# Kernel tuning notes

Measured on AMD Instinct MI355X. Metric: run time of the kernel, lower is better.

Reference implementation:

```python
import jax, jax.numpy as jnp
import numpy as np

NEG_SLOPE = 0.2
EPS = 1e-16
N_NODES, N_EDGES, N_GRAPHS = 50000, 800000, 64
EMB, HID, HEADS = 128, 64, 4


def segment_softmax(scores, seg, num_segments):
    # scores: [E, H], seg: [E] destination ids
    m = jax.ops.segment_max(scores, seg, num_segments=num_segments)
    e = jnp.exp(scores - m[seg])
    s = jax.ops.segment_sum(e, seg, num_segments=num_segments)
    return e / (s[seg] + EPS)


def gat_layer(x, edge_index, W, att_src, att_dst, bias, heads, out_ch, num_nodes):
    # PyG GATConv (add_self_loops handled by caller): linear -> per-edge attn -> segment softmax -> scatter-add
    h = (x @ W).reshape(num_nodes, heads, out_ch)          # [N, H, C]
    a_src = jnp.sum(h * att_src, axis=-1)                  # [N, H]
    a_dst = jnp.sum(h * att_dst, axis=-1)                  # [N, H]
    src, dst = edge_index[0], edge_index[1]
    alpha = jax.nn.leaky_relu(a_src[src] + a_dst[dst], NEG_SLOPE)   # [E, H]
    alpha = segment_softmax(alpha, dst, num_nodes)
    msg = h[src] * alpha[:, :, None]                       # [E, H, C]
    out = jax.ops.segment_sum(msg, dst, num_segments=num_nodes)
    return out.reshape(num_nodes, heads * out_ch) + bias


def setup_inputs() -> dict:
    key = jax.random.key(0)
    ks = jax.random.split(key, 16)
    g = lambda k, shape, fan: jax.random.normal(k, shape, jnp.float32) * (1.0 / np.sqrt(fan))
    x = jax.random.normal(ks[0], (N_NODES, EMB), jnp.float32)
    edge_index = jax.random.randint(ks[1], (2, N_EDGES), 0, N_NODES, dtype=jnp.int64)
    batch_map = jnp.sort(jax.random.randint(ks[2], (N_NODES,), 0, N_GRAPHS, dtype=jnp.int64))
    return {
        'x': x, 'edge_index': edge_index, 'batch_map': batch_map,
        'W1': g(ks[3], (EMB, HEADS * HID), EMB),
        'att_src1': g(ks[4], (HEADS, HID), HID),
        'att_dst1': g(ks[5], (HEADS, HID), HID),
        'b1': jnp.zeros((HEADS * HID,), jnp.float32),
        'W2': g(ks[6], (HEADS * HID, HID), HEADS * HID),
        'att_src2': g(ks[7], (1, HID), HID),
        'att_dst2': g(ks[8], (1, HID), HID),
        'b2': jnp.zeros((HID,), jnp.float32),
        'Wg1': g(ks[9], (HID, HID), HID),
        'bg1': jnp.zeros((HID,), jnp.float32),
        'Wg2': g(ks[10], (HID, 1), HID),
        'bg2': jnp.zeros((1,), jnp.float32),
    }


def reference(x, edge_index, batch_map, W1, att_src1, att_dst1, b1, W2, att_src2, att_dst2, b2, Wg1, bg1, Wg2, bg2):
    n = x.shape[0]
    # GATConv default add_self_loops=True
    loops = jnp.arange(n, dtype=edge_index.dtype)
    ei = jnp.concatenate([edge_index, jnp.stack([loops, loops])], axis=1)
    h = jax.nn.elu(gat_layer(x, ei, W1, att_src1, att_dst1, b1, HEADS, HID, n))
    h = jax.nn.elu(gat_layer(h, ei, W2, att_src2, att_dst2, b2, 1, HID, n))
    # AttentionalAggregation: gate MLP -> segment softmax over graphs -> weighted sum
    gate = jax.nn.relu(h @ Wg1 + bg1) @ Wg2 + bg2          # [N, 1]
    w = segment_softmax(gate, batch_map, N_GRAPHS)         # [N, 1]
    graph_emb = jax.ops.segment_sum(w * h, batch_map, num_segments=N_GRAPHS)
    return graph_emb
```

## Files before the change

### kernel.cpp

```cpp
#include <hip/hip_runtime.h>
#include <math.h>

#define N_NODES 50000
#define N_EDGES 800000
#define E_TOT   850000
#define N_GRAPHS 64
#define EMB 128
#define HID 64
#define HEADS 4
#define NEG_SLOPE 0.2f
#define EPS 1e-16f
#define MAX_DEG 64
#define G1_TILES (N_NODES / 16)
#define ELL_BLKS ((E_TOT + 255) / 256)

typedef short bf16x8 __attribute__((ext_vector_type(8)));
typedef float f32x4  __attribute__((ext_vector_type(4)));

__device__ __forceinline__ float leaky(float x) { return x >= 0.f ? x : NEG_SLOPE * x; }
__device__ __forceinline__ float elu(float x)   { return x > 0.f ? x : expf(x) - 1.f; }

__device__ __forceinline__ unsigned short f2bf(float f) {
    unsigned u = __float_as_uint(f);
    return (unsigned short)((u + 0x7FFFu + ((u >> 16) & 1u)) >> 16);
}
__device__ __forceinline__ float bf2f(unsigned short h) {
    return __uint_as_float((unsigned)h << 16);
}

__device__ __forceinline__ void edge_sd(const int* __restrict__ ei, int e, int& s, int& d) {
    if (e < N_EDGES) { s = ei[e]; d = ei[N_EDGES + e]; }
    else             { s = d = e - N_EDGES; }
}

__device__ __forceinline__ int lbound(const int* __restrict__ a, int n, int v) {
    int lo = 0, hi = n;
    while (lo < hi) { int mid = (lo + hi) >> 1; if (a[mid] < v) lo = mid + 1; else hi = mid; }
    return lo;
}

__global__ void k_wprep(const float* __restrict__ W1, const float* __restrict__ as1, const float* __restrict__ ad1,
                        const float* __restrict__ W2, const float* __restrict__ as2, const float* __restrict__ ad2,
                        const float* __restrict__ Wg1,
                        unsigned short* __restrict__ W1t, float* __restrict__ v1s, float* __restrict__ v1d,
                        unsigned short* __restrict__ W2t, float* __restrict__ v2s, float* __restrict__ v2d,
                        unsigned short* __restrict__ wg1h, unsigned short* __restrict__ wg1l,
                        unsigned* __restrict__ cnt) {
    int b = blockIdx.x, t = threadIdx.x;
    if (b < 32) {
        for (int i = b * 1024 + t; i < (b + 1) * 1024; i += 256) {
            int c = i >> 7, k = i & 127;
            W1t[i] = f2bf(W1[k * 256 + c]);
        }
    } else if (b < 48) {
        int bb = b - 32;
        for (int i = bb * 1024 + t; i < (bb + 1) * 1024; i += 256) {
            int c = i >> 8, k = i & 255;
            W2t[i] = f2bf(W2[k * 64 + c]);
        }
    } else if (b == 48) {
        for (int i = t; i < 512; i += 256) {
            int h = i >> 7, k = i & 127;
            float s = 0.f, d = 0.f;
            for (int c = 0; c < 64; ++c) {
                float wv = W1[k * 256 + h * 64 + c];
                s = fmaf(wv, as1[h * 64 + c], s);
                d = fmaf(wv, ad1[h * 64 + c], d);
            }
            v1s[i] = s; v1d[i] = d;
        }
    } else if (b == 49) {
        float s = 0.f, d = 0.f;
        for (int cc = 0; cc < 64; ++cc) {
            float wv = W2[t * 64 + cc];
            s = fmaf(wv, as2[cc], s);
            d = fmaf(wv, ad2[cc], d);
        }
        v2s[t] = s; v2d[t] = d;
    } else if (b == 50) {
        for (int i = t; i < 4096; i += 256) {
            int c = i >> 6, k = i & 63;
            float v = Wg1[k * 64 + c];
            unsigned short h = f2bf(v);
            wg1h[i] = h;
            wg1l[i] = f2bf(v - bf2f(h));
        }
    } else {
        for (int i = (b - 51) * 256 + t; i < N_NODES; i += 13 * 256) cnt[i] = 0;
    }
}

__global__ __launch_bounds__(256)
void k_prep2(const float* __restrict__ x, const unsigned short* __restrict__ W1t,
             const float* __restrict__ v1s, const float* __restrict__ v1d,
             unsigned short* __restrict__ h1b, float* __restrict__ a_src1,
             float* __restrict__ a_dst1,
             const int* __restrict__ ei, unsigned* __restrict__ cnt,
             unsigned short* __restrict__ ell) {
    if (blockIdx.x >= G1_TILES) {
        int e = (blockIdx.x - G1_TILES) * 256 + threadIdx.x;
        if (e < E_TOT) {
            int s, d; edge_sd(ei, e, s, d);
            unsigned slot = atomicAdd(&cnt[d], 1u);
            if (slot < MAX_DEG) ell[d * MAX_DEG + slot] = (unsigned short)s;
        }
        return;
    }
    int w = threadIdx.x >> 6, l = threadIdx.x & 63;
    int r = l & 15, kg = l >> 4;
    int tile = blockIdx.x;
    const float* xr = x + (size_t)(tile * 16 + r) * 128 + kg * 8;
    bf16x8 af[4];
    float ps = 0.f, pd = 0.f;
    #pragma unroll
    for (int j = 0; j < 4; ++j) {
        float4 f0 = *(const float4*)(xr + j * 32);
        float4 f1 = *(const float4*)(xr + j * 32 + 4);
        const float* vs = v1s + w * 128 + j * 32 + kg * 8;
        const float* vd = v1d + w * 128 + j * 32 + kg * 8;
        float4 s0 = *(const float4*)vs, s1 = *(const float4*)(vs + 4);
        float4 d0 = *(const float4*)vd, d1 = *(const float4*)(vd + 4);
        ps += f0.x*s0.x + f0.y*s0.y + f0.z*s0.z + f0.w*s0.w
            + f1.x*s1.x + f1.y*s1.y + f1.z*s1.z + f1.w*s1.w;
        pd += f0.x*d0.x + f0.y*d0.y + f0.z*d0.z + f0.w*d0.w
            + f1.x*d1.x + f1.y*d1.y + f1.z*d1.z + f1.w*d1.w;
        bf16x8 t;
        t[0] = (short)f2bf(f0.x); t[1] = (short)f2bf(f0.y);
        t[2] = (short)f2bf(f0.z); t[3] = (short)f2bf(f0.w);
        t[4] = (short)f2bf(f1.x); t[5] = (short)f2bf(f1.y);
        t[6] = (short)f2bf(f1.z); t[7] = (short)f2bf(f1.w);
        af[j] = t;
    }
    ps += __shfl_xor(ps, 16); ps += __shfl_xor(ps, 32);
    pd += __shfl_xor(pd, 16); pd += __shfl_xor(pd, 32);
    if (l < 16) {
        a_src1[(size_t)(tile * 16 + r) * 4 + w] = ps;
        a_dst1[(size_t)(tile * 16 + r) * 4 + w] = pd;
    }
    for (int cc = 0; cc < 4; ++cc) {
        int c0 = cc * 64 + w * 16;
        const bf16x8* B = (const bf16x8*)(W1t + (size_t)(c0 + r) * 128 + kg * 8);
        f32x4 acc = {0.f, 0.f, 0.f, 0.f};
        acc = __builtin_amdgcn_mfma_f32_16x16x32_bf16(af[0], B[0],  acc, 0, 0, 0);
        acc = __builtin_amdgcn_mfma_f32_16x16x32_bf16(af[1], B[4],  acc, 0, 0, 0);
        acc = __builtin_amdgcn_mfma_f32_16x16x32_bf16(af[2], B[8],  acc, 0, 0, 0);
        acc = __builtin_amdgcn_mfma_f32_16x16x32_bf16(af[3], B[12], acc, 0, 0, 0);
        #pragma unroll
        for (int j = 0; j < 4; ++j)
            h1b[(size_t)(tile * 16 + kg * 4 + j) * 256 + c0 + r] = f2bf(acc[j]);
    }
}

__global__ __launch_bounds__(1024)
void k_layer1(const unsigned short* __restrict__ ell, const unsigned* __restrict__ cnt,
              const float4* __restrict__ asrc, const float4* __restrict__ adst,
              const unsigned short* __restrict__ h1b, const float4* __restrict__ bias,
              const float4* __restrict__ v2s4, const float4* __restrict__ v2d4,
              const unsigned short* __restrict__ W2t,
              float* __restrict__ a_src2, float* __restrict__ a_dst2,
              unsigned short* __restrict__ h2b) {
    __shared__ float sw[4][16][65];
    __shared__ int   ss[16][MAX_DEG];
    __shared__ unsigned short Ash[16][264];
    int wave = threadIdx.x >> 6, lane = threadIdx.x & 63;
    int node = blockIdx.x * 16 + wave;
    int deg = min((int)cnt[node], MAX_DEG);

    float4 ad = adst[node];
    float a0 = -INFINITY, a1 = -INFINITY, a2 = -INFINITY, a3 = -INFINITY;
    int s = 0;
    if (lane < deg) {
        s = ell[node * MAX_DEG + lane];
        float4 as = asrc[s];
        a0 = leaky(as.x + ad.x); a1 = leaky(as.y + ad.y);
        a2 = leaky(as.z + ad.z); a3 = leaky(as.w + ad.w);
    }
    float m0 = a0, m1 = a1, m2 = a2, m3 = a3;
    for (int o = 32; o > 0; o >>= 1) {
        m0 = fmaxf(m0, __shfl_xor(m0, o)); m1 = fmaxf(m1, __shfl_xor(m1, o));
        m2 = fmaxf(m2, __shfl_xor(m2, o)); m3 = fmaxf(m3, __shfl_xor(m3, o));
    }
    float w0 = lane < deg ? expf(a0 - m0) : 0.f;
    float w1 = lane < deg ? expf(a1 - m1) : 0.f;
    float w2 = lane < deg ? expf(a2 - m2) : 0.f;
    float w3 = lane < deg ? expf(a3 - m3) : 0.f;
    float t0 = w0, t1 = w1, t2 = w2, t3 = w3;
    for (int o = 32; o > 0; o >>= 1) {
        t0 += __shfl_xor(t0, o); t1 += __shfl_xor(t1, o);
        t2 += __shfl_xor(t2, o); t3 += __shfl_xor(t3, o);
    }
    w0 /= (t0 + EPS); w1 /= (t1 + EPS); w2 /= (t2 + EPS); w3 /= (t3 + EPS);
    if (lane < deg) {
        sw[0][wave][lane] = w0; sw[1][wave][lane] = w1;
        sw[2][wave][lane] = w2; sw[3][wave][lane] = w3;
        ss[wave][lane] = s;
    }
    int head = lane >> 4;
    float c0 = 0.f, c1 = 0.f, c2 = 0.f, c3 = 0.f;
    ushort4 hcur = *(const ushort4*)(h1b + (size_t)ss[wave][0] * 256 + lane * 4);
    float   wcur = sw[head][wave][0];
    for (int e = 1; e < deg; ++e) {
        ushort4 hnx = *(const ushort4*)(h1b + (size_t)ss[wave][e] * 256 + lane * 4);
        float   wnx = sw[head][wave][e];
        c0 = fmaf(bf2f(hcur.x), wcur, c0); c1 = fmaf(bf2f(hcur.y), wcur, c1);
        c2 = fmaf(bf2f(hcur.z), wcur, c2); c3 = fmaf(bf2f(hcur.w), wcur, c3);
        hcur = hnx; wcur = wnx;
    }
    c0 = fmaf(bf2f(hcur.x), wcur, c0); c1 = fmaf(bf2f(hcur.y), wcur, c1);
    c2 = fmaf(bf2f(hcur.z), wcur, c2); c3 = fmaf(bf2f(hcur.w), wcur, c3);

    float4 b = bias[lane];
    float o0 = elu(c0 + b.x), o1 = elu(c1 + b.y), o2 = elu(c2 + b.z), o3 = elu(c3 + b.w);
    *(ushort4*)&Ash[wave][lane * 4] = make_ushort4(f2bf(o0), f2bf(o1), f2bf(o2), f2bf(o3));
    float4 vs = v2s4[lane], vd = v2d4[lane];
    float ps = o0 * vs.x + o1 * vs.y + o2 * vs.z + o3 * vs.w;
    float pd = o0 * vd.x + o1 * vd.y + o2 * vd.z + o3 * vd.w;
    for (int o = 32; o > 0; o >>= 1) { ps += __shfl_xor(ps, o); pd += __shfl_xor(pd, o); }
    if (lane == 0) { a_src2[node] = ps; a_dst2[node] = pd; }

    __syncthreads();
    if (wave < 4) {
        int r = lane & 15, kg = lane >> 4;
        f32x4 acc = {0.f, 0.f, 0.f, 0.f};
        #pragma unroll
        for (int kk = 0; kk < 8; ++kk) {
            bf16x8 afr = *(const bf16x8*)&Ash[r][kg * 8 + kk * 32];
            bf16x8 bfr = *(const bf16x8*)(W2t + (size_t)(wave * 16 + r) * 256 + kg * 8 + kk * 32);
            acc = __builtin_amdgcn_mfma_f32_16x16x32_bf16(afr, bfr, acc, 0, 0, 0);
        }
        #pragma unroll
        for (int j = 0; j < 4; ++j)
            h2b[(size_t)(blockIdx.x * 16 + kg * 4 + j) * 64 + wave * 16 + r] = f2bf(acc[j]);
    }
}

__global__ __launch_bounds__(1024)
void k_layer2(const unsigned short* __restrict__ ell, const unsigned* __restrict__ cnt,
              const float* __restrict__ asrc, const float* __restrict__ adst,
              const unsigned short* __restrict__ h2b, const float* __restrict__ bias,
              const unsigned short* __restrict__ wg1h, const unsigned short* __restrict__ wg1l,
              const float* __restrict__ bg1, const float* __restrict__ Wg2,
              const float* __restrict__ bg2,
              float* __restrict__ out2, float* __restrict__ gate) {
    __shared__ float sw[16][MAX_DEG];
    __shared__ int   ss[16][MAX_DEG];
    __shared__ unsigned short Ah[16][72], Al[16][72];
    __shared__ float gp[4][16];
    int wave = threadIdx.x >> 6, lane = threadIdx.x & 63;
    int half = lane >> 5, li = lane & 31;
    int node = blockIdx.x * 16 + wave;
    int deg = min((int)cnt[node], MAX_DEG);

    float adv = adst[node];
    float a = -INFINITY;
    int s = 0;
    if (lane < deg) {
        s = ell[node * MAX_DEG + lane];
        a = leaky(asrc[s] + adv);
    }
    float m = a;
    for (int o = 32; o > 0; o >>= 1) m = fmaxf(m, __shfl_xor(m, o));
    float w = lane < deg ? expf(a - m) : 0.f;
    float t = w;
    for (int o = 32; o > 0; o >>= 1) t += __shfl_xor(t, o);
    w /= (t + EPS);
    if (lane < deg) { sw[wave][lane] = w; ss[wave][lane] = s; }

    float c0 = 0.f, c1 = 0.f;
    int row = half;
    unsigned ucur = 0; float wcur = 0.f;
    if (row < deg) {
        ucur = *(const unsigned*)(h2b + (size_t)ss[wave][row] * 64 + li * 2);
        wcur = sw[wave][row];
    }
    while (row < deg) {
        int nrow = row + 2;
        unsigned unx = 0; float wnx = 0.f;
        if (nrow < deg) {
            unx = *(const unsigned*)(h2b + (size_t)ss[wave][nrow] * 64 + li * 2);
            wnx = sw[wave][nrow];
        }
        c0 = fmaf(__uint_as_float(ucur << 16), wcur, c0);
        c1 = fmaf(__uint_as_float(ucur & 0xffff0000u), wcur, c1);
        ucur = unx; wcur = wnx; row = nrow;
    }
    c0 += __shfl_xor(c0, 32);
    c1 += __shfl_xor(c1, 32);
    if (half == 0) {
        float o0 = elu(c0 + bias[li * 2]);
        float o1 = elu(c1 + bias[li * 2 + 1]);
        *(float2*)(out2 + (size_t)node * 64 + li * 2) = make_float2(o0, o1);
        unsigned short h0 = f2bf(o0), h1 = f2bf(o1);
        *(unsigned*)&Ah[wave][li * 2] = ((unsigned)h1 << 16) | h0;
        unsigned short l0 = f2bf(o0 - bf2f(h0)), l1 = f2bf(o1 - bf2f(h1));
        *(unsigned*)&Al[wave][li * 2] = ((unsigned)l1 << 16) | l0;
    }

    __syncthreads();
    if (wave < 4) {
        int r = lane & 15, kg = lane >> 4;
        const bf16x8* Bh = (const bf16x8*)(wg1h + (size_t)(wave * 16 + r) * 64 + kg * 8);
        const bf16x8* Bl = (const bf16x8*)(wg1l + (size_t)(wave * 16 + r) * 64 + kg * 8);
        bf16x8 ah0 = *(const bf16x8*)&Ah[r][kg * 8];
        bf16x8 ah1 = *(const bf16x8*)&Ah[r][kg * 8 + 32];
        bf16x8 al0 = *(const bf16x8*)&Al[r][kg * 8];
        bf16x8 al1 = *(const bf16x8*)&Al[r][kg * 8 + 32];
        f32x4 acc = {0.f, 0.f, 0.f, 0.f};
        acc = __builtin_amdgcn_mfma_f32_16x16x32_bf16(ah0, Bh[0], acc, 0, 0, 0);
        acc = __builtin_amdgcn_mfma_f32_16x16x32_bf16(ah1, Bh[4], acc, 0, 0, 0);
        acc = __builtin_amdgcn_mfma_f32_16x16x32_bf16(ah0, Bl[0], acc, 0, 0, 0);
        acc = __builtin_amdgcn_mfma_f32_16x16x32_bf16(ah1, Bl[4], acc, 0, 0, 0);
        acc = __builtin_amdgcn_mfma_f32_16x16x32_bf16(al0, Bh[0], acc, 0, 0, 0);
        acc = __builtin_amdgcn_mfma_f32_16x16x32_bf16(al1, Bh[4], acc, 0, 0, 0);
        int col = wave * 16 + r;
        float wg2 = Wg2[col], bb = bg1[col];
        float part[4];
        #pragma unroll
        for (int j = 0; j < 4; ++j) part[j] = fmaxf(acc[j] + bb, 0.f) * wg2;
        #pragma unroll
        for (int o = 8; o > 0; o >>= 1) {
            #pragma unroll
            for (int j = 0; j < 4; ++j) part[j] += __shfl_xor(part[j], o);
        }
        if (r == 0) {
            #pragma unroll
            for (int j = 0; j < 4; ++j) gp[wave][kg * 4 + j] = part[j];
        }
    }
    __syncthreads();
    if (threadIdx.x < 16)
        gate[blockIdx.x * 16 + threadIdx.x] = gp[0][threadIdx.x] + gp[1][threadIdx.x]
                                            + gp[2][threadIdx.x] + gp[3][threadIdx.x] + bg2[0];
}

__global__ __launch_bounds__(1024)
void k_final(const float* __restrict__ gate, const float* __restrict__ hfin,
             const int* __restrict__ batch, float* __restrict__ out) {
    __shared__ float red[16];
    __shared__ float redc[16][64];
    int g = blockIdx.x;
    int lo = lbound(batch, N_NODES, g);
    int hi = lbound(batch, N_NODES, g + 1);
    int tid = threadIdx.x, wave = tid >> 6, lane = tid & 63;

    float m = -INFINITY;
    for (int i = lo + tid; i < hi; i += 1024) m = fmaxf(m, gate[i]);
    for (int o = 32; o > 0; o >>= 1) m = fmaxf(m, __shfl_xor(m, o));
    if (lane == 0) red[wave] = m;
    __syncthreads();
    m = -INFINITY;
    #pragma unroll
    for (int i = 0; i < 16; ++i) m = fmaxf(m, red[i]);
    __syncthreads();

    float s = 0.f;
    for (int i = lo + tid; i < hi; i += 1024) s += expf(gate[i] - m);
    for (int o = 32; o > 0; o >>= 1) s += __shfl_xor(s, o);
    if (lane == 0) red[wave] = s;
    __syncthreads();
    s = 0.f;
    #pragma unroll
    for (int i = 0; i < 16; ++i) s += red[i];

    float acc = 0.f;
    for (int i = lo + wave; i < hi; i += 16)
        acc = fmaf(expf(gate[i] - m), hfin[(size_t)i * 64 + lane], acc);
    redc[wave][lane] = acc;
    __syncthreads();
    if (tid < 64) {
        float r = 0.f;
        #pragma unroll
        for (int i = 0; i < 16; ++i) r += redc[i][tid];
        out[g * 64 + tid] = r / (s + EPS);
    }
}

extern "C" void kernel_launch(void* const* d_in, const int* in_sizes, int n_in,
                              void* d_out, int out_size, void* d_ws, size_t ws_size,
                              hipStream_t stream) {
    const float* x    = (const float*)d_in[0];
    const int*   ei   = (const int*)d_in[1];
    const int*   batch= (const int*)d_in[2];
    const float* W1   = (const float*)d_in[3];
    const float* as1  = (const float*)d_in[4];
    const float* ad1  = (const float*)d_in[5];
    const float* b1   = (const float*)d_in[6];
    const float* W2   = (const float*)d_in[7];
    const float* as2  = (const float*)d_in[8];
    const float* ad2  = (const float*)d_in[9];
    const float* b2   = (const float*)d_in[10];
    const float* Wg1  = (const float*)d_in[11];
    const float* bg1  = (const float*)d_in[12];
    const float* Wg2  = (const float*)d_in[13];
    const float* bg2  = (const float*)d_in[14];
    float* out = (float*)d_out;

    char* W = (char*)d_ws;
    size_t off = 0;
    unsigned* cnt = (unsigned*)(W + off); off += (size_t)N_NODES * 4;
    unsigned short* ell  = (unsigned short*)(W + off); off += (size_t)N_NODES * MAX_DEG * 2;
    unsigned short* h1b  = (unsigned short*)(W + off); off += (size_t)N_NODES * 256 * 2;
    float* a_src1 = (float*)(W + off); off += (size_t)N_NODES * HEADS * 4;
    float* a_dst1 = (float*)(W + off); off += (size_t)N_NODES * HEADS * 4;
    float* a_src2 = (float*)(W + off); off += (size_t)N_NODES * 4;
    float* a_dst2 = (float*)(W + off); off += (size_t)N_NODES * 4;
    float* out2   = (float*)(W + off); off += (size_t)N_NODES * HID * 4;
    float* gate   = (float*)(W + off); off += (size_t)N_NODES * 4;
    unsigned short* W1t = (unsigned short*)(W + off); off += (size_t)128 * 256 * 2;
    float* v1s = (float*)(W + off); off += 512 * 4;
    float* v1d = (float*)(W + off); off += 512 * 4;
    unsigned short* W2t = (unsigned short*)(W + off); off += (size_t)64 * 256 * 2;
    float* v2s = (float*)(W + off); off += 256 * 4;
    float* v2d = (float*)(W + off); off += 256 * 4;
    unsigned short* wg1h = (unsigned short*)(W + off); off += (size_t)64 * 64 * 2;
    unsigned short* wg1l = (unsigned short*)(W + off); off += (size_t)64 * 64 * 2;
    unsigned short* h2b = (unsigned short*)(W + off); off += (size_t)N_NODES * HID * 2;
    (void)ws_size; (void)in_sizes; (void)n_in; (void)out_size;

    k_wprep<<<64, 256, 0, stream>>>(W1, as1, ad1, W2, as2, ad2, Wg1,
                                    W1t, v1s, v1d, W2t, v2s, v2d, wg1h, wg1l, cnt);
    k_prep2<<<G1_TILES + ELL_BLKS, 256, 0, stream>>>(x, W1t, v1s, v1d, h1b, a_src1, a_dst1,
                                                     ei, cnt, ell);
    k_layer1<<<N_NODES / 16, 1024, 0, stream>>>(ell, cnt, (const float4*)a_src1,
        (const float4*)a_dst1, h1b, (const float4*)b1,
        (const float4*)v2s, (const float4*)v2d, W2t, a_src2, a_dst2, h2b);
    k_layer2<<<N_NODES / 16, 1024, 0, stream>>>(ell, cnt, a_src2, a_dst2, h2b, b2,
                                                wg1h, wg1l, bg1, Wg2, bg2, out2, gate);
    k_final<<<N_GRAPHS, 1024, 0, stream>>>(gate, out2, batch, out);
}
```

Measured before the change: 282.6 us.

## Build ELL adjacency with per-block LDS atomics over owned node ranges

The ELL neighbour-list build moves out of the fused GEMM/scatter kernel into a dedicated kernel with 64 blocks. Each block owns a contiguous slice of destination nodes, scans every edge's destination, and claims slots with shared-memory atomics instead of global atomics. Self-loops are written directly as slot 0, so the separate zeroing of the global count array goes away. The cost is that every block reads the whole destination array and only 64 blocks run, which underuses the GPU; the ELL build also no longer overlaps with the first GEMM.

```diff
diff --git a/kernel.cpp b/kernel.cpp
--- a/kernel.cpp
+++ b/kernel.cpp
@@ -11,8 +11,8 @@
 #define NEG_SLOPE 0.2f
 #define EPS 1e-16f
 #define MAX_DEG 64
-#define G1_TILES (N_NODES / 16)
-#define ELL_BLKS ((E_TOT + 255) / 256)
+#define ELL_NB 64
+#define ELL_NODES ((N_NODES + ELL_NB - 1) / ELL_NB)
 
 typedef short bf16x8 __attribute__((ext_vector_type(8)));
 typedef float f32x4  __attribute__((ext_vector_type(4)));
@@ -26,17 +26,38 @@
 }
 __device__ __forceinline__ float bf2f(unsigned short h) {
     return __uint_as_float((unsigned)h << 16);
-}
-
-__device__ __forceinline__ void edge_sd(const int* __restrict__ ei, int e, int& s, int& d) {
-    if (e < N_EDGES) { s = ei[e]; d = ei[N_EDGES + e]; }
-    else             { s = d = e - N_EDGES; }
 }
 
 __device__ __forceinline__ int lbound(const int* __restrict__ a, int n, int v) {
     int lo = 0, hi = n;
     while (lo < hi) { int mid = (lo + hi) >> 1; if (a[mid] < v) lo = mid + 1; else hi = mid; }
     return lo;
+}
+
+__global__ __launch_bounds__(1024)
+void k_ell2(const int* __restrict__ ei, unsigned* __restrict__ cnt,
+            unsigned short* __restrict__ ell) {
+    __shared__ unsigned lcnt[ELL_NODES];
+    int base = blockIdx.x * ELL_NODES;
+    int nOwn = min(base + ELL_NODES, N_NODES) - base;
+    for (int i = threadIdx.x; i < nOwn; i += 1024) {
+        lcnt[i] = 1;
+        ell[(size_t)(base + i) * MAX_DEG] = (unsigned short)(base + i);
+    }
+    __syncthreads();
+    const int* dsts = ei + N_EDGES;
+    for (int e = threadIdx.x; e < N_EDGES; e += 1024) {
+        int d = dsts[e];
+        unsigned rel = (unsigned)(d - base);
+        if (rel < (unsigned)nOwn) {
+            unsigned slot = atomicAdd(&lcnt[rel], 1u);
+            if (slot < MAX_DEG)
+                ell[(size_t)d * MAX_DEG + slot] = (unsigned short)ei[e];
+        }
+    }
+    __syncthreads();
+    for (int i = threadIdx.x; i < nOwn; i += 1024)
+        cnt[base + i] = lcnt[i];
 }
 
 __global__ void k_wprep(const float* __restrict__ W1, const float* __restrict__ as1, const float* __restrict__ ad1,
@@ -44,8 +65,7 @@
                         const float* __restrict__ Wg1,
                         unsigned short* __restrict__ W1t, float* __restrict__ v1s, float* __restrict__ v1d,
                         unsigned short* __restrict__ W2t, float* __restrict__ v2s, float* __restrict__ v2d,
-                        unsigned short* __restrict__ wg1h, unsigned short* __restrict__ wg1l,
-                        unsigned* __restrict__ cnt) {
+                        unsigned short* __restrict__ wg1h, unsigned short* __restrict__ wg1l) {
     int b = blockIdx.x, t = threadIdx.x;
     if (b < 32) {
         for (int i = b * 1024 + t; i < (b + 1) * 1024; i += 256) {
@@ -77,7 +97,7 @@
             d = fmaf(wv, ad2[cc], d);
         }
         v2s[t] = s; v2d[t] = d;
-    } else if (b == 50) {
+    } else {
         for (int i = t; i < 4096; i += 256) {
             int c = i >> 6, k = i & 63;
             float v = Wg1[k * 64 + c];
@@ -85,27 +105,14 @@
             wg1h[i] = h;
             wg1l[i] = f2bf(v - bf2f(h));
         }
-    } else {
-        for (int i = (b - 51) * 256 + t; i < N_NODES; i += 13 * 256) cnt[i] = 0;
     }
 }
 
 __global__ __launch_bounds__(256)
-void k_prep2(const float* __restrict__ x, const unsigned short* __restrict__ W1t,
-             const float* __restrict__ v1s, const float* __restrict__ v1d,
-             unsigned short* __restrict__ h1b, float* __restrict__ a_src1,
-             float* __restrict__ a_dst1,
-             const int* __restrict__ ei, unsigned* __restrict__ cnt,
-             unsigned short* __restrict__ ell) {
-    if (blockIdx.x >= G1_TILES) {
-        int e = (blockIdx.x - G1_TILES) * 256 + threadIdx.x;
-        if (e < E_TOT) {
-            int s, d; edge_sd(ei, e, s, d);
-            unsigned slot = atomicAdd(&cnt[d], 1u);
-            if (slot < MAX_DEG) ell[d * MAX_DEG + slot] = (unsigned short)s;
-        }
-        return;
-    }
+void k_gemm1_mfma(const float* __restrict__ x, const unsigned short* __restrict__ W1t,
+                  const float* __restrict__ v1s, const float* __restrict__ v1d,
+                  unsigned short* __restrict__ h1b, float* __restrict__ a_src1,
+                  float* __restrict__ a_dst1) {
     int w = threadIdx.x >> 6, l = threadIdx.x & 63;
     int r = l & 15, kg = l >> 4;
     int tile = blockIdx.x;
@@ -417,10 +424,10 @@
     unsigned short* h2b = (unsigned short*)(W + off); off += (size_t)N_NODES * HID * 2;
     (void)ws_size; (void)in_sizes; (void)n_in; (void)out_size;
 
-    k_wprep<<<64, 256, 0, stream>>>(W1, as1, ad1, W2, as2, ad2, Wg1,
-                                    W1t, v1s, v1d, W2t, v2s, v2d, wg1h, wg1l, cnt);
-    k_prep2<<<G1_TILES + ELL_BLKS, 256, 0, stream>>>(x, W1t, v1s, v1d, h1b, a_src1, a_dst1,
-                                                     ei, cnt, ell);
+    k_ell2<<<ELL_NB, 1024, 0, stream>>>(ei, cnt, ell);
+    k_wprep<<<51, 256, 0, stream>>>(W1, as1, ad1, W2, as2, ad2, Wg1,
+                                    W1t, v1s, v1d, W2t, v2s, v2d, wg1h, wg1l);
+    k_gemm1_mfma<<<N_NODES / 16, 256, 0, stream>>>(x, W1t, v1s, v1d, h1b, a_src1, a_dst1);
     k_layer1<<<N_NODES / 16, 1024, 0, stream>>>(ell, cnt, (const float4*)a_src1,
         (const float4*)a_dst1, h1b, (const float4*)b1,
         (const float4*)v2s, (const float4*)v2d, W2t, a_src2, a_dst2, h2b);
```

Result: slower. 579.9 us (+105.2%).

## Split per-node edge counters into four sub-buckets and compact into ELL

Applied to the files above, without the earlier changes.

Edges are spread over four sub-counters per destination node, chosen by edge index mod 4, so atomic contention on each counter drops. A new compaction kernel then merges the sub-buckets into the dense ELL layout. This adds an extra kernel launch, more workspace traffic and a larger zero-init. Each sub-bucket is capped at 20 entries, so a node whose edges are unevenly spread can drop edges that the single 64-slot counter would have kept.

```diff
diff --git a/kernel.cpp b/kernel.cpp
--- a/kernel.cpp
+++ b/kernel.cpp
@@ -11,6 +11,7 @@
 #define NEG_SLOPE 0.2f
 #define EPS 1e-16f
 #define MAX_DEG 64
+#define SUB_CAP 20
 #define G1_TILES (N_NODES / 16)
 #define ELL_BLKS ((E_TOT + 255) / 256)
 
@@ -45,7 +46,7 @@
                         unsigned short* __restrict__ W1t, float* __restrict__ v1s, float* __restrict__ v1d,
                         unsigned short* __restrict__ W2t, float* __restrict__ v2s, float* __restrict__ v2d,
                         unsigned short* __restrict__ wg1h, unsigned short* __restrict__ wg1l,
-                        unsigned* __restrict__ cnt) {
+                        unsigned* __restrict__ cnt4) {
     int b = blockIdx.x, t = threadIdx.x;
     if (b < 32) {
         for (int i = b * 1024 + t; i < (b + 1) * 1024; i += 256) {
@@ -86,7 +87,7 @@
             wg1l[i] = f2bf(v - bf2f(h));
         }
     } else {
-        for (int i = (b - 51) * 256 + t; i < N_NODES; i += 13 * 256) cnt[i] = 0;
+        for (int i = (b - 51) * 256 + t; i < 4 * N_NODES; i += 13 * 256) cnt4[i] = 0;
     }
 }
 
@@ -95,14 +96,16 @@
              const float* __restrict__ v1s, const float* __restrict__ v1d,
              unsigned short* __restrict__ h1b, float* __restrict__ a_src1,
              float* __restrict__ a_dst1,
-             const int* __restrict__ ei, unsigned* __restrict__ cnt,
-             unsigned short* __restrict__ ell) {
+             const int* __restrict__ ei, unsigned* __restrict__ cnt4,
+             unsigned short* __restrict__ ell4) {
     if (blockIdx.x >= G1_TILES) {
         int e = (blockIdx.x - G1_TILES) * 256 + threadIdx.x;
         if (e < E_TOT) {
             int s, d; edge_sd(ei, e, s, d);
-            unsigned slot = atomicAdd(&cnt[d], 1u);
-            if (slot < MAX_DEG) ell[d * MAX_DEG + slot] = (unsigned short)s;
+            int sub = e & 3;
+            unsigned slot = atomicAdd(&cnt4[sub * N_NODES + d], 1u);
+            if (slot < SUB_CAP)
+                ell4[(size_t)d * (4 * SUB_CAP) + sub * SUB_CAP + slot] = (unsigned short)s;
         }
         return;
     }
@@ -151,6 +154,24 @@
     }
 }
 
+__global__ __launch_bounds__(256)
+void k_compact(const unsigned* __restrict__ cnt4, const unsigned short* __restrict__ ell4,
+               unsigned* __restrict__ cnt, unsigned short* __restrict__ ell) {
+    int n = blockIdx.x * 256 + threadIdx.x;
+    if (n >= N_NODES) return;
+    int pos = 0;
+    #pragma unroll
+    for (int sub = 0; sub < 4; ++sub) {
+        int c = min((int)cnt4[sub * N_NODES + n], SUB_CAP);
+        for (int k = 0; k < c; ++k) {
+            if (pos < MAX_DEG)
+                ell[(size_t)n * MAX_DEG + pos] = ell4[(size_t)n * (4 * SUB_CAP) + sub * SUB_CAP + k];
+            ++pos;
+        }
+    }
+    cnt[n] = min(pos, MAX_DEG);
+}
+
 __global__ __launch_bounds__(1024)
 void k_layer1(const unsigned short* __restrict__ ell, const unsigned* __restrict__ cnt,
               const float4* __restrict__ asrc, const float4* __restrict__ adst,
@@ -397,8 +418,10 @@
 
     char* W = (char*)d_ws;
     size_t off = 0;
-    unsigned* cnt = (unsigned*)(W + off); off += (size_t)N_NODES * 4;
+    unsigned* cnt  = (unsigned*)(W + off); off += (size_t)N_NODES * 4;
+    unsigned* cnt4 = (unsigned*)(W + off); off += (size_t)4 * N_NODES * 4;
     unsigned short* ell  = (unsigned short*)(W + off); off += (size_t)N_NODES * MAX_DEG * 2;
+    unsigned short* ell4 = (unsigned short*)(W + off); off += (size_t)N_NODES * 4 * SUB_CAP * 2;
     unsigned short* h1b  = (unsigned short*)(W + off); off += (size_t)N_NODES * 256 * 2;
     float* a_src1 = (float*)(W + off); off += (size_t)N_NODES * HEADS * 4;
     float* a_dst1 = (float*)(W + off); off += (size_t)N_NODES * HEADS * 4;
@@ -418,9 +441,10 @@
     (void)ws_size; (void)in_sizes; (void)n_in; (void)out_size;
 
     k_wprep<<<64, 256, 0, stream>>>(W1, as1, ad1, W2, as2, ad2, Wg1,
-                                    W1t, v1s, v1d, W2t, v2s, v2d, wg1h, wg1l, cnt);
+                                    W1t, v1s, v1d, W2t, v2s, v2d, wg1h, wg1l, cnt4);
     k_prep2<<<G1_TILES + ELL_BLKS, 256, 0, stream>>>(x, W1t, v1s, v1d, h1b, a_src1, a_dst1,
-                                                     ei, cnt, ell);
+                                                     ei, cnt4, ell4);
+    k_compact<<<(N_NODES + 255) / 256, 256, 0, stream>>>(cnt4, ell4, cnt, ell);
     k_layer1<<<N_NODES / 16, 1024, 0, stream>>>(ell, cnt, (const float4*)a_src1,
         (const float4*)a_dst1, h1b, (const float4*)b1,
         (const float4*)v2s, (const float4*)v2d, W2t, a_src2, a_dst2, h2b);
```

Result: slower. 294.1 us (+4.1%).
